# Performance work log

Measured on AMD Instinct MI355X. Metric: run time of the kernel, lower is better.

Reference implementation:

```python
import jax, jax.numpy as jnp
import numpy as np

D = 192          # embed_dim
DI = 2 * D       # d_inner (Mamba expand=2)
R = 12           # dt_rank = ceil(D / d_state)
N = 16           # d_state
DEPTH = 24
P = 16           # patch size
B = 4
SS, TS = 256, 128
PT = (TS // P) ** 2   # 64 template patches
PS = (SS // P) ** 2   # 256 search patches
L = PT + PS + 1       # 321 tokens (middle cls)


def setup_inputs() -> dict:
    key = jax.random.key(0)
    ks = jax.random.split(key, 24)
    f = lambda k, shp, s=0.02: (jax.random.normal(k, shp) * s).astype(jnp.float32)
    Alog = jnp.log(jnp.arange(1, N + 1, dtype=jnp.float32))  # S4D-real init
    Alog = jnp.tile(Alog, (DEPTH, DI, 1))
    return {
        "x_search": f(ks[0], (B, 3, SS, SS), 1.0),
        "x_template": f(ks[1], (B, 3, TS, TS), 1.0),
        "patch_w": f(ks[2], (D, 3, P, P)),
        "patch_b": jnp.zeros((D,), jnp.float32),
        "cls_token": f(ks[3], (1, 1, D)),
        "pos_embed": f(ks[4], (1, L, D)),
        "Win": f(ks[5], (DEPTH, 2 * DI, D)),
        "convw": f(ks[6], (DEPTH, DI, 4), 0.2),
        "convb": jnp.zeros((DEPTH, DI), jnp.float32),
        "Wx": f(ks[7], (DEPTH, R + 2 * N, DI)),
        "Wdt": f(ks[8], (DEPTH, DI, R), 0.1),
        "bdt": f(ks[9], (DEPTH, DI), 0.1),
        "Alog": Alog,
        "Dp": jnp.ones((DEPTH, DI), jnp.float32),
        "convw_b": f(ks[10], (DEPTH, DI, 4), 0.2),
        "convb_b": jnp.zeros((DEPTH, DI), jnp.float32),
        "Wx_b": f(ks[11], (DEPTH, R + 2 * N, DI)),
        "Wdt_b": f(ks[12], (DEPTH, DI, R), 0.1),
        "bdt_b": f(ks[13], (DEPTH, DI), 0.1),
        "Alog_b": Alog,
        "Dp_b": jnp.ones((DEPTH, DI), jnp.float32),
        "Wout": f(ks[14], (DEPTH, D, DI)),
        "normw": jnp.ones((DEPTH, D), jnp.float32),
        "normw_f": jnp.ones((D,), jnp.float32),
    }


def silu(x):
    return x * jax.nn.sigmoid(x)


def rmsnorm(x, w, eps=1e-5):
    return x * jax.lax.rsqrt(jnp.mean(x * x, -1, keepdims=True) + eps) * w


def patch_embed(x, w, b):
    # non-overlapping patch conv == blocked reshape + einsum
    Bn, C, H, W = x.shape
    xp = x.reshape(Bn, C, H // P, P, W // P, P)
    t = jnp.einsum('bcipjq,dcpq->bijd', xp, w)
    return t.reshape(Bn, (H // P) * (W // P), -1) + b


def causal_conv(u, w, b):
    # depthwise causal conv, kernel 4: u [B,DI,L], w [DI,4]
    Lx = u.shape[-1]
    up = jnp.pad(u, ((0, 0), (0, 0), (3, 0)))
    y = sum(w[:, k][None, :, None] * up[:, :, k:k + Lx] for k in range(4))
    return y + b[None, :, None]


def selective_scan(u, delta, A, Bm, Cm, Dp):
    # u, delta: [B,DI,L]; A: [DI,N]; Bm, Cm: [B,N,L]
    dA = jnp.exp(jnp.einsum('bdl,dn->lbdn', delta, A))
    dBu = jnp.einsum('bdl,bnl->lbdn', delta * u, Bm)

    def step(h, inp):
        dAt, dBut, ct = inp
        h = dAt * h + dBut
        return h, jnp.einsum('bdn,bn->bd', h, ct)

    h0 = jnp.zeros((u.shape[0], DI, N), u.dtype)
    _, ys = jax.lax.scan(step, h0, (dA, dBu, Cm.transpose(2, 0, 1)))
    y = ys.transpose(1, 2, 0)  # [B,DI,L]
    return y + Dp[None, :, None] * u


def _branch(x, z, convw, convb, Wx, Wdt, bdt, Alog, Dp):
    xc = silu(causal_conv(x, convw, convb))
    xdbl = jnp.einsum('bdl,ed->ble', xc, Wx)
    dt, Bm, Cm = xdbl[..., :R], xdbl[..., R:R + N], xdbl[..., R + N:]
    delta = jax.nn.softplus(jnp.einsum('blr,dr->bdl', dt, Wdt) + bdt[None, :, None])
    y = selective_scan(xc, delta, -jnp.exp(Alog), Bm.transpose(0, 2, 1),
                       Cm.transpose(0, 2, 1), Dp)
    return y * silu(z)


def _mixer(h, p):
    xz = jnp.einsum('bld,ed->ble', h, p['Win'])
    x = xz[..., :DI].transpose(0, 2, 1)   # [B,DI,L]
    z = xz[..., DI:].transpose(0, 2, 1)
    y = _branch(x, z, p['convw'], p['convb'], p['Wx'], p['Wdt'], p['bdt'],
                p['Alog'], p['Dp'])
    yb = _branch(x[..., ::-1], z[..., ::-1], p['convw_b'], p['convb_b'], p['Wx_b'],
                 p['Wdt_b'], p['bdt_b'], p['Alog_b'], p['Dp_b'])
    out = (y + yb[..., ::-1]) * 0.5  # bimamba v2 with if_divide_out
    return jnp.einsum('bdl,od->blo', out, p['Wout'])


def reference(x_search, x_template, patch_w, patch_b, cls_token, pos_embed,
              Win, convw, convb, Wx, Wdt, bdt, Alog, Dp,
              convw_b, convb_b, Wx_b, Wdt_b, bdt_b, Alog_b, Dp_b,
              Wout, normw, normw_f):
    ts = patch_embed(x_template, patch_w, patch_b)   # [B,64,D]
    ss = patch_embed(x_search, patch_w, patch_b)     # [B,256,D]
    tok = jnp.concatenate([ts, ss], 1)               # [B,320,D]
    mid = tok.shape[1] // 2
    cls = jnp.broadcast_to(cls_token, (tok.shape[0], 1, D))
    tok = jnp.concatenate([tok[:, :mid], cls, tok[:, mid:]], 1) + pos_embed

    lp = {'Win': Win, 'convw': convw, 'convb': convb, 'Wx': Wx, 'Wdt': Wdt,
          'bdt': bdt, 'Alog': Alog, 'Dp': Dp, 'convw_b': convw_b,
          'convb_b': convb_b, 'Wx_b': Wx_b, 'Wdt_b': Wdt_b, 'bdt_b': bdt_b,
          'Alog_b': Alog_b, 'Dp_b': Dp_b, 'Wout': Wout, 'normw': normw}

    def layer_step(carry, p):
        hidden, residual = carry
        residual = hidden + residual           # add
        hn = rmsnorm(residual, p['normw'])     # norm (fused_add_norm semantics)
        hidden = _mixer(hn, p)                 # mamba mixer
        return (hidden, residual), None

    (hidden, residual), _ = jax.lax.scan(layer_step, (tok, jnp.zeros_like(tok)), lp)
    return rmsnorm(hidden + residual, normw_f)   # final add + norm, [B,321,D]
```

## Files before the change

kernel.cpp:

```cpp
#include <hip/hip_runtime.h>
#include <math.h>

#define B_ 4
#define L_ 321
#define D_ 192
#define DI_ 384
#define E_ 768
#define R_ 12
#define N_ 16
#define DEPTH_ 24
#define XD 44

#define NC_ 21
#define LC_ 16

typedef __attribute__((ext_vector_type(8))) short bf16x8;
typedef __attribute__((ext_vector_type(4))) float f32x4;
typedef unsigned short ushort_t;

__device__ __forceinline__ float silu_f(float x) { return x / (1.f + __expf(-x)); }

__device__ __forceinline__ ushort_t f2bf(float x) {
    union { float f; unsigned u; } v; v.f = x;
    return (ushort_t)((v.u + 0x7fffu + ((v.u >> 16) & 1u)) >> 16);
}
__device__ __forceinline__ float bf2f(ushort_t h) {
    union { unsigned u; float f; } v; v.u = ((unsigned)h) << 16; return v.f;
}

__global__ void cvt_bf16_multi(const float* __restrict__ s0, ushort_t* __restrict__ d0, int n0,
                               const float* __restrict__ s1, ushort_t* __restrict__ d1, int n1,
                               const float* __restrict__ s2, ushort_t* __restrict__ d2, int n2,
                               const float* __restrict__ s3, ushort_t* __restrict__ d3, int n3,
                               const float* __restrict__ s4, ushort_t* __restrict__ d4, int n4) {
    int total = n0 + n1 + n2 + n3 + n4;
    for (int i = blockIdx.x * blockDim.x + threadIdx.x; i < total; i += gridDim.x * blockDim.x) {
        int j = i;
        const float* s; ushort_t* d;
        if (j < n0) { s = s0; d = d0; }
        else { j -= n0;
            if (j < n1) { s = s1; d = d1; }
            else { j -= n1;
                if (j < n2) { s = s2; d = d2; }
                else { j -= n2;
                    if (j < n3) { s = s3; d = d3; }
                    else { j -= n3; s = s4; d = d4; }
                }
            }
        }
        d[j] = f2bf(s[j]);
    }
}

__global__ void im2col_kernel(const float* __restrict__ xs, const float* __restrict__ xt,
                              ushort_t* __restrict__ pm) {
    int p_all = blockIdx.x % 320;
    int b = blockIdx.x / 320;
    const float* src; int i, j, W;
    if (p_all < 64) { int p = p_all; i = p >> 3; j = p & 7; W = 128; src = xt + (size_t)b*3*128*128; }
    else            { int p = p_all - 64; i = p >> 4; j = p & 15; W = 256; src = xs + (size_t)b*3*256*256; }
    ushort_t* dst = pm + (size_t)blockIdx.x * 768;
    for (int m = threadIdx.x; m < 768; m += blockDim.x) {
        int c = m >> 8, rem = m & 255, pp = rem >> 4, qq = rem & 15;
        dst[m] = f2bf(src[(size_t)(c*W + i*16 + pp)*W + j*16 + qq]);
    }
}

__global__ void tok_rms(const float* __restrict__ tokmat, const float* __restrict__ pb,
                        const float* __restrict__ cls, const float* __restrict__ pos,
                        const float* __restrict__ normw,
                        float* __restrict__ residual, ushort_t* __restrict__ hn) {
    int blk = blockIdx.x;
    int b = blk / L_, t = blk % L_;
    int d = threadIdx.x;
    float v;
    if (t == 160) v = cls[d];
    else {
        int p = (t < 160) ? t : t - 1;
        v = tokmat[(size_t)(b*320 + p)*D_ + d] + pb[d];
    }
    v += pos[t*D_ + d];
    residual[(size_t)blk*D_ + d] = v;
    float sq = v * v;
#pragma unroll
    for (int m = 1; m < 64; m <<= 1) sq += __shfl_xor(sq, m, 64);
    __shared__ float part[3];
    int wave = d >> 6, lane = d & 63;
    if (lane == 0) part[wave] = sq;
    __syncthreads();
    float tot = part[0] + part[1] + part[2];
    float scale = rsqrtf(tot / (float)D_ + 1e-5f);
    hn[(size_t)blk*D_ + d] = f2bf(v * scale * normw[d]);
}

template<int WM, int WN, int MFR, int NFR, int CMODE, int KK>
__global__ __launch_bounds__(WM*WN*64) void mfma_gemm(const ushort_t* __restrict__ A,
                          const ushort_t* __restrict__ Bw,
                          float* __restrict__ Cf, ushort_t* __restrict__ Ch,
                          int M, int N) {
    constexpr int BM = WM * MFR * 16;
    constexpr int BN = WN * NFR * 16;
    int bx = blockIdx.x, by = blockIdx.y;
    int wave = threadIdx.x >> 6, lane = threadIdx.x & 63;
    int wr = wave / WN, wc = wave % WN;
    int m0 = by * BM + wr * MFR * 16;
    int n0 = bx * BN + wc * NFR * 16;
    int lrow = lane & 15;
    int lk   = (lane >> 4) * 8;

    f32x4 acc[MFR][NFR];
#pragma unroll
    for (int i = 0; i < MFR; ++i)
#pragma unroll
        for (int j = 0; j < NFR; ++j) acc[i][j] = (f32x4){0.f, 0.f, 0.f, 0.f};

#pragma unroll 6
    for (int k0 = 0; k0 < KK; k0 += 32) {
        bf16x8 a[MFR], b[NFR];
#pragma unroll
        for (int i = 0; i < MFR; ++i) {
            int r = m0 + i*16 + lrow; r = min(r, M - 1);
            a[i] = *(const bf16x8*)(A + (size_t)r*KK + k0 + lk);
        }
#pragma unroll
        for (int jn = 0; jn < NFR; ++jn) {
            int c = n0 + jn*16 + lrow; c = min(c, N - 1);
            b[jn] = *(const bf16x8*)(Bw + (size_t)c*KK + k0 + lk);
        }
#pragma unroll
        for (int i = 0; i < MFR; ++i)
#pragma unroll
            for (int jn = 0; jn < NFR; ++jn)
                acc[i][jn] = __builtin_amdgcn_mfma_f32_16x16x32_bf16(a[i], b[jn], acc[i][jn], 0, 0, 0);
    }

    int crow = (lane >> 4) * 4;
    int ccol = lane & 15;
#pragma unroll
    for (int i = 0; i < MFR; ++i)
#pragma unroll
        for (int jn = 0; jn < NFR; ++jn) {
            int c = n0 + jn*16 + ccol;
            if (c >= N) continue;
#pragma unroll
            for (int j = 0; j < 4; ++j) {
                int r = m0 + i*16 + crow + j;
                if (r < M) {
                    if (CMODE == 0) Cf[(size_t)r*N + c] = acc[i][jn][j];
                    else            Ch[(size_t)r*N + c] = f2bf(acc[i][jn][j]);
                }
            }
        }
}

__global__ __launch_bounds__(384) void scan1_conv(
    const ushort_t* __restrict__ xzb,
    const ushort_t* __restrict__ Wxf, const ushort_t* __restrict__ Wxbw,
    const float* __restrict__ cw, const float* __restrict__ cb,
    const float* __restrict__ cwb, const float* __restrict__ cbb,
    const float* __restrict__ Wdt, const float* __restrict__ bdt,
    const float* __restrict__ Wdtb, const float* __restrict__ bdtb,
    const float* __restrict__ Alog, const float* __restrict__ Alogb,
    ushort_t* __restrict__ xc_f, ushort_t* __restrict__ xc_b,
    float* __restrict__ xdbl_f, float* __restrict__ xdbl_b,
    float* __restrict__ hloc, float* __restrict__ aprod) {
    int c = blockIdx.x, b = blockIdx.y, br = blockIdx.z;
    int tid = threadIdx.x, wave = tid >> 6, lane = tid & 63;
    const ushort_t* Wx = br ? Wxbw : Wxf;
    const float* cwp = br ? cwb : cw;
    const float* cbp = br ? cbb : cb;
    const float* Wd = br ? Wdtb : Wdt;
    const float* bd = br ? bdtb : bdt;
    const float* Al = br ? Alogb : Alog;
    ushort_t* xcout = br ? xc_b : xc_f;
    float* xdout = br ? xdbl_b : xdbl_f;

    __shared__ ushort_t sxc[LC_][DI_ + 8];
    __shared__ float sxd[LC_][48];
    int lbeg = c * LC_;
    int len = min(lbeg + LC_, L_) - lbeg;
    int d = tid;

    float4 w4 = *(const float4*)(cwp + (size_t)d*4);
    float b0 = cbp[d];
    const ushort_t* xrow = xzb + (size_t)b*L_*E_ + d;
    float u[LC_];
    if (len == LC_) {
        float xr[LC_ + 3];
#pragma unroll
        for (int t2 = 0; t2 < LC_ + 3; ++t2) {
            int t = lbeg - 3 + t2;
            float v = 0.f;
            if (t >= 0) { int tr = br ? (L_ - 1 - t) : t; v = bf2f(xrow[(size_t)tr*E_]); }
            xr[t2] = v;
        }
#pragma unroll
        for (int l2 = 0; l2 < LC_; ++l2) {
            float acc = b0;
            acc = fmaf(w4.x, xr[l2 + 0], acc);
            acc = fmaf(w4.y, xr[l2 + 1], acc);
            acc = fmaf(w4.z, xr[l2 + 2], acc);
            acc = fmaf(w4.w, xr[l2 + 3], acc);
            ushort_t hv = f2bf(silu_f(acc));
            sxc[l2][d] = hv;
            u[l2] = bf2f(hv);
            xcout[((size_t)b*L_ + lbeg + l2)*DI_ + d] = hv;
        }
    } else {
        for (int l2 = 0; l2 < len; ++l2) {
            int l = lbeg + l2;
            float acc = b0;
#pragma unroll
            for (int k = 0; k < 4; ++k) {
                int t = l - 3 + k;
                if (t >= 0) {
                    int tr = br ? (L_ - 1 - t) : t;
                    acc = fmaf(((const float*)&w4)[k], bf2f(xrow[(size_t)tr*E_]), acc);
                }
            }
            ushort_t hv = f2bf(silu_f(acc));
            sxc[l2][d] = hv;
            u[l2] = bf2f(hv);
            xcout[((size_t)b*L_ + lbeg + l2)*DI_ + d] = hv;
        }
    }
    __syncthreads();

    if (wave < 3) {
        int lrow = lane & 15, lk = (lane >> 4) * 8;
        int ar = min(lrow, len - 1);
        int bcol = min(wave * 16 + lrow, XD - 1);
        f32x4 acc = (f32x4){0.f, 0.f, 0.f, 0.f};
#pragma unroll
        for (int k0 = 0; k0 < DI_; k0 += 32) {
            bf16x8 a  = *(const bf16x8*)(&sxc[ar][k0 + lk]);
            bf16x8 bw = *(const bf16x8*)(Wx + (size_t)bcol * DI_ + k0 + lk);
            acc = __builtin_amdgcn_mfma_f32_16x16x32_bf16(a, bw, acc, 0, 0, 0);
        }
        int crow = (lane >> 4) * 4, ccol = lane & 15;
#pragma unroll
        for (int j = 0; j < 4; ++j) sxd[crow + j][wave * 16 + ccol] = acc[j];
    }
    __syncthreads();

    for (int idx = tid; idx < len * XD; idx += 384) {
        int l2 = idx / XD, col = idx % XD;
        xdout[((size_t)b*L_ + lbeg + l2)*XD + col] = sxd[l2][col];
    }

    float wreg[R_];
#pragma unroll
    for (int r = 0; r < R_; ++r) wreg[r] = Wd[d*R_ + r];
    float bdv = bd[d];
    float a[N_];
#pragma unroll
    for (int n = 0; n < N_; ++n) a[n] = -__expf(Al[d*N_ + n]);
    float h[N_], ap[N_];
#pragma unroll
    for (int n = 0; n < N_; ++n) { h[n] = 0.f; ap[n] = 1.f; }

    auto step = [&](int l2, float uv) {
        float dacc = bdv;
#pragma unroll
        for (int r = 0; r < R_; ++r) dacc = fmaf(wreg[r], sxd[l2][r], dacc);
        float dv = fmaxf(dacc, 0.f) + log1pf(__expf(-fabsf(dacc)));
        float du = dv * uv;
#pragma unroll
        for (int n = 0; n < N_; ++n) {
            float e = __expf(dv * a[n]);
            h[n] = fmaf(e, h[n], du * sxd[l2][R_ + n]);
            ap[n] *= e;
        }
    };
    if (len == LC_) {
#pragma unroll 4
        for (int l2 = 0; l2 < LC_; ++l2) step(l2, u[l2]);
    } else {
        for (int l2 = 0; l2 < len; ++l2) step(l2, u[l2]);
    }
    size_t base = (((size_t)(b*2 + br)*NC_ + c)*N_)*DI_ + d;
#pragma unroll
    for (int n = 0; n < N_; ++n) {
        hloc[base + (size_t)n*DI_]  = h[n];
        aprod[base + (size_t)n*DI_] = ap[n];
    }
}

__global__ void scan_combine(const float* __restrict__ hloc, const float* __restrict__ aprod,
                             float* __restrict__ hin) {
    int g = blockIdx.x * blockDim.x + threadIdx.x;
    int bb = g / (N_ * DI_);
    int rem = g % (N_ * DI_);
    float hrun = 0.f;
#pragma unroll
    for (int c = 0; c < NC_; ++c) {
        size_t idx = ((size_t)bb*NC_ + c)*N_*DI_ + rem;
        hin[idx] = hrun;
        hrun = fmaf(aprod[idx], hrun, hloc[idx]);
    }
}

__global__ __launch_bounds__(192) void scan_part3(
                           const ushort_t* __restrict__ xc_f, const ushort_t* __restrict__ xc_b,
                           const float* __restrict__ xdbl_f, const float* __restrict__ xdbl_b,
                           const float* __restrict__ Wdt, const float* __restrict__ bdt,
                           const float* __restrict__ Wdtb, const float* __restrict__ bdtb,
                           const ushort_t* __restrict__ xz,
                           const float* __restrict__ Alog, const float* __restrict__ Alogb,
                           const float* __restrict__ Dpf, const float* __restrict__ Dpb,
                           const float* __restrict__ hin,
                           ushort_t* __restrict__ y_f, ushort_t* __restrict__ y_b) {
    int c = blockIdx.x, b = blockIdx.y >> 1, half = blockIdx.y & 1, br = blockIdx.z;
    int tid = threadIdx.x;
    int d = half * 192 + tid;
    const ushort_t* xc = br ? xc_b : xc_f;
    const float* xd = br ? xdbl_b : xdbl_f;
    const float* Wd = br ? Wdtb : Wdt;
    const float* bd = br ? bdtb : bdt;
    const float* Al = br ? Alogb : Alog;
    const float* Dpp = br ? Dpb : Dpf;
    ushort_t* y = br ? y_b : y_f;
    __shared__ float sdt[LC_][R_];
    __shared__ float sB[LC_][N_];
    __shared__ float sC[LC_][N_];
    int lbeg = c * LC_;
    int len = min(lbeg + LC_, L_) - lbeg;
    for (int idx = tid; idx < len*N_; idx += 192) {
        int l2 = idx >> 4, n = idx & 15;
        size_t row = (size_t)b*L_ + lbeg + l2;
        sB[l2][n] = xd[row*XD + R_ + n];
        sC[l2][n] = xd[row*XD + R_ + N_ + n];
    }
    for (int idx = tid; idx < len*R_; idx += 192) {
        int l2 = idx / R_, r = idx % R_;
        sdt[l2][r] = xd[((size_t)b*L_ + lbeg + l2)*XD + r];
    }
    __syncthreads();
    float wreg[R_];
#pragma unroll
    for (int r = 0; r < R_; ++r) wreg[r] = Wd[d*R_ + r];
    float bdv = bd[d];
    float a[N_];
#pragma unroll
    for (int n = 0; n < N_; ++n) a[n] = -__expf(Al[d*N_ + n]);
    float h[N_];
    size_t hbase = (((size_t)(b*2 + br)*NC_ + c)*N_)*DI_ + d;
#pragma unroll
    for (int n = 0; n < N_; ++n) h[n] = hin[hbase + (size_t)n*DI_];
    float dpv = Dpp[d];

    auto step = [&](int l2, float uv) {
        float dacc = bdv;
#pragma unroll
        for (int r = 0; r < R_; ++r) dacc = fmaf(wreg[r], sdt[l2][r], dacc);
        float dv = fmaxf(dacc, 0.f) + log1pf(__expf(-fabsf(dacc)));
        float du = dv * uv;
        float yv = 0.f;
#pragma unroll
        for (int n = 0; n < N_; ++n) {
            float e = __expf(dv * a[n]);
            h[n] = fmaf(e, h[n], du * sB[l2][n]);
            yv = fmaf(h[n], sC[l2][n], yv);
        }
        yv = fmaf(dpv, uv, yv);
        int lo = br ? (L_ - 1 - (lbeg + l2)) : (lbeg + l2);
        float zv = bf2f(xz[((size_t)b*L_ + lo)*E_ + DI_ + d]);
        y[((size_t)b*L_ + lo)*DI_ + d] = f2bf(yv * silu_f(zv));
    };
    if (len == LC_) {
        float u[LC_];
#pragma unroll
        for (int l2 = 0; l2 < LC_; ++l2)
            u[l2] = bf2f(xc[((size_t)b*L_ + lbeg + l2)*DI_ + d]);
#pragma unroll 4
        for (int l2 = 0; l2 < LC_; ++l2) step(l2, u[l2]);
    } else {
        for (int l2 = 0; l2 < len; ++l2)
            step(l2, bf2f(xc[((size_t)b*L_ + lbeg + l2)*DI_ + d]));
    }
}

template<bool LAST>
__global__ __launch_bounds__(256) void outproj_fused(
    const ushort_t* __restrict__ yf, const ushort_t* __restrict__ yb,
    const ushort_t* __restrict__ Ww,
    float* __restrict__ residual, const float* __restrict__ nw,
    ushort_t* __restrict__ hn, float* __restrict__ outp) {
    const int M = B_*L_, Nn = D_, K = DI_;
    int wave = threadIdx.x >> 6, lane = threadIdx.x & 63;
    int m0 = blockIdx.x * 16;
    int n0 = wave * 48;
    int lrow = lane & 15, lk = (lane >> 4) * 8;

    f32x4 acc[3];
#pragma unroll
    for (int jn = 0; jn < 3; ++jn) acc[jn] = (f32x4){0.f, 0.f, 0.f, 0.f};

#pragma unroll 4
    for (int k0 = 0; k0 < K; k0 += 32) {
        int r = min(m0 + lrow, M - 1);
        bf16x8 vf = *(const bf16x8*)(yf + (size_t)r*K + k0 + lk);
        bf16x8 vb = *(const bf16x8*)(yb + (size_t)r*K + k0 + lk);
        bf16x8 a;
#pragma unroll
        for (int j = 0; j < 8; ++j)
            a[j] = (short)f2bf(0.5f*(bf2f((ushort_t)vf[j]) + bf2f((ushort_t)vb[j])));
        bf16x8 b[3];
#pragma unroll
        for (int jn = 0; jn < 3; ++jn) {
            int c = n0 + jn*16 + lrow;
            b[jn] = *(const bf16x8*)(Ww + (size_t)c*K + k0 + lk);
        }
#pragma unroll
        for (int jn = 0; jn < 3; ++jn)
            acc[jn] = __builtin_amdgcn_mfma_f32_16x16x32_bf16(a, b[jn], acc[jn], 0, 0, 0);
    }

    int crow = (lane >> 4) * 4, ccol = lane & 15;
    float resv[4][3];
    float sq[4] = {0.f, 0.f, 0.f, 0.f};
#pragma unroll
    for (int j = 0; j < 4; ++j) {
        int r = m0 + crow + j;
        bool ok = r < M;
#pragma unroll
        for (int jn = 0; jn < 3; ++jn) {
            int c = n0 + jn*16 + ccol;
            float v = ok ? (residual[(size_t)r*Nn + c] + acc[jn][j]) : 0.f;
            resv[j][jn] = v;
            sq[j] = fmaf(v, v, sq[j]);
        }
    }
#pragma unroll
    for (int m = 1; m < 16; m <<= 1)
#pragma unroll
        for (int j = 0; j < 4; ++j) sq[j] += __shfl_xor(sq[j], m, 64);

    __shared__ float part[16][4];
    if (ccol == 0) {
#pragma unroll
        for (int j = 0; j < 4; ++j) part[crow + j][wave] = sq[j];
    }
    __syncthreads();
#pragma unroll
    for (int j = 0; j < 4; ++j) {
        int r = m0 + crow + j;
        if (r >= M) continue;
        int rt = crow + j;
        float tot = part[rt][0] + part[rt][1] + part[rt][2] + part[rt][3];
        float scale = rsqrtf(tot / (float)Nn + 1e-5f);
#pragma unroll
        for (int jn = 0; jn < 3; ++jn) {
            int c = n0 + jn*16 + ccol;
            float v = resv[j][jn];
            if (LAST) {
                outp[(size_t)r*Nn + c] = v * scale * nw[c];
            } else {
                residual[(size_t)r*Nn + c] = v;
                hn[(size_t)r*Nn + c] = f2bf(v * scale * nw[c]);
            }
        }
    }
}

extern "C" void kernel_launch(void* const* d_in, const int* in_sizes, int n_in,
                              void* d_out, int out_size, void* d_ws, size_t ws_size,
                              hipStream_t stream) {
    const float* xs     = (const float*)d_in[0];
    const float* xt     = (const float*)d_in[1];
    const float* pw     = (const float*)d_in[2];
    const float* pb     = (const float*)d_in[3];
    const float* cls    = (const float*)d_in[4];
    const float* pos    = (const float*)d_in[5];
    const float* Win    = (const float*)d_in[6];
    const float* convw  = (const float*)d_in[7];
    const float* convb  = (const float*)d_in[8];
    const float* Wx     = (const float*)d_in[9];
    const float* Wdt    = (const float*)d_in[10];
    const float* bdt    = (const float*)d_in[11];
    const float* Alog   = (const float*)d_in[12];
    const float* Dp     = (const float*)d_in[13];
    const float* convwb = (const float*)d_in[14];
    const float* convbb = (const float*)d_in[15];
    const float* Wxb    = (const float*)d_in[16];
    const float* Wdtb   = (const float*)d_in[17];
    const float* bdtb   = (const float*)d_in[18];
    const float* Alogb  = (const float*)d_in[19];
    const float* Dpb    = (const float*)d_in[20];
    const float* Wout   = (const float*)d_in[21];
    const float* normw  = (const float*)d_in[22];
    const float* normwf = (const float*)d_in[23];
    float* out = (float*)d_out;

    float* ws = (float*)d_ws;
    size_t off = 0;
    auto alloc = [&](size_t nfloats) { float* p = ws + off; off += nfloats; return p; };
    const size_t BL = (size_t)B_ * L_;
    const size_t CHNK = (size_t)B_ * 2 * NC_ * N_ * DI_;

    float*    residual = alloc(BL * D_);
    ushort_t* hn_bf    = (ushort_t*)alloc(BL * D_ / 2);
    ushort_t* xzb_bf   = (ushort_t*)alloc(BL * E_ / 2);
    ushort_t* xcf_bf   = (ushort_t*)alloc(BL * DI_ / 2);
    ushort_t* xcb_bf   = (ushort_t*)alloc(BL * DI_ / 2);
    float*    xdbl_f   = alloc(BL * XD);
    float*    xdbl_b   = alloc(BL * XD);
    ushort_t* y_f      = (ushort_t*)alloc(BL * DI_ / 2);
    ushort_t* y_b      = (ushort_t*)alloc(BL * DI_ / 2);
    float*    hloc     = alloc(CHNK);
    float*    aprod    = alloc(CHNK);
    float*    hin      = alloc(CHNK);
    ushort_t* pw_bf    = (ushort_t*)alloc((size_t)D_ * 768 / 2);
    ushort_t* Win_bf   = (ushort_t*)alloc((size_t)DEPTH_ * E_ * D_ / 2);
    ushort_t* Wx_bf    = (ushort_t*)alloc((size_t)DEPTH_ * XD * DI_ / 2);
    ushort_t* Wxb_bf   = (ushort_t*)alloc((size_t)DEPTH_ * XD * DI_ / 2);
    ushort_t* Wout_bf  = (ushort_t*)alloc((size_t)DEPTH_ * D_ * DI_ / 2);
    (void)ws_size; (void)in_sizes; (void)n_in; (void)out_size;

    cvt_bf16_multi<<<dim3(2048), dim3(256), 0, stream>>>(
        pw,   pw_bf,   D_ * 768,
        Win,  Win_bf,  DEPTH_ * E_ * D_,
        Wx,   Wx_bf,   DEPTH_ * XD * DI_,
        Wxb,  Wxb_bf,  DEPTH_ * XD * DI_,
        Wout, Wout_bf, DEPTH_ * D_ * DI_);

    ushort_t* pmat   = (ushort_t*)hloc;
    float*    tokmat = aprod;
    im2col_kernel<<<dim3(B_ * 320), dim3(256), 0, stream>>>(xs, xt, pmat);
    mfma_gemm<2, 2, 2, 2, 0, 768><<<dim3(3, 20), dim3(256), 0, stream>>>(
        pmat, pw_bf, tokmat, nullptr, B_ * 320, D_);
    tok_rms<<<dim3(B_ * L_), dim3(192), 0, stream>>>(tokmat, pb, cls, pos, normw, residual, hn_bf);

    for (int layer = 0; layer < DEPTH_; ++layer) {
        const ushort_t* Win_l  = Win_bf  + (size_t)layer * E_ * D_;
        const ushort_t* Wx_l   = Wx_bf   + (size_t)layer * XD * DI_;
        const ushort_t* Wxb_l  = Wxb_bf  + (size_t)layer * XD * DI_;
        const ushort_t* Wout_l = Wout_bf + (size_t)layer * D_ * DI_;
        const float* cw_l    = convw  + (size_t)layer * DI_ * 4;
        const float* cb_l    = convb  + (size_t)layer * DI_;
        const float* cwb_l   = convwb + (size_t)layer * DI_ * 4;
        const float* cbb_l   = convbb + (size_t)layer * DI_;
        const float* Wdt_l   = Wdt    + (size_t)layer * DI_ * R_;
        const float* Wdtb_l  = Wdtb   + (size_t)layer * DI_ * R_;
        const float* bdt_l   = bdt    + (size_t)layer * DI_;
        const float* bdtb_l  = bdtb   + (size_t)layer * DI_;
        const float* Alog_l  = Alog   + (size_t)layer * DI_ * N_;
        const float* Alogb_l = Alogb  + (size_t)layer * DI_ * N_;
        const float* Dp_l    = Dp     + (size_t)layer * DI_;
        const float* Dpb_l   = Dpb    + (size_t)layer * DI_;

        mfma_gemm<2, 2, 2, 2, 1, 192><<<dim3(12, 21), dim3(256), 0, stream>>>(
            hn_bf, Win_l, nullptr, xzb_bf, (int)BL, E_);
        scan1_conv<<<dim3(NC_, B_, 2), dim3(384), 0, stream>>>(
            xzb_bf, Wx_l, Wxb_l, cw_l, cb_l, cwb_l, cbb_l,
            Wdt_l, bdt_l, Wdtb_l, bdtb_l, Alog_l, Alogb_l,
            xcf_bf, xcb_bf, xdbl_f, xdbl_b, hloc, aprod);
        scan_combine<<<dim3((B_*2*N_*DI_)/256), dim3(256), 0, stream>>>(hloc, aprod, hin);
        scan_part3<<<dim3(NC_, B_ * 2, 2), dim3(192), 0, stream>>>(
            xcf_bf, xcb_bf, xdbl_f, xdbl_b, Wdt_l, bdt_l, Wdtb_l, bdtb_l, xzb_bf,
            Alog_l, Alogb_l, Dp_l, Dpb_l, hin, y_f, y_b);
        if (layer < DEPTH_ - 1) {
            outproj_fused<false><<<dim3(81), dim3(256), 0, stream>>>(
                y_f, y_b, Wout_l, residual, normw + (size_t)(layer + 1) * D_, hn_bf, nullptr);
        } else {
            outproj_fused<true><<<dim3(81), dim3(256), 0, stream>>>(
                y_f, y_b, Wout_l, residual, normwf, nullptr, out);
        }
    }
}
```

Baseline: 1.746 ms.

## Fuse next layer's in-projection GEMM into out-projection/residual-norm kernel

```diff
diff --git a/kernel.cpp b/kernel.cpp
--- a/kernel.cpp
+++ b/kernel.cpp
@@ -381,52 +381,55 @@
 }
 
 template<bool LAST>
-__global__ __launch_bounds__(256) void outproj_fused(
+__global__ __launch_bounds__(384) void outproj_inproj(
     const ushort_t* __restrict__ yf, const ushort_t* __restrict__ yb,
     const ushort_t* __restrict__ Ww,
+    const ushort_t* __restrict__ Win_next,
     float* __restrict__ residual, const float* __restrict__ nw,
-    ushort_t* __restrict__ hn, float* __restrict__ outp) {
-    const int M = B_*L_, Nn = D_, K = DI_;
+    ushort_t* __restrict__ xzb_out, float* __restrict__ outp) {
+    const int M = B_*L_;
     int wave = threadIdx.x >> 6, lane = threadIdx.x & 63;
     int m0 = blockIdx.x * 16;
-    int n0 = wave * 48;
     int lrow = lane & 15, lk = (lane >> 4) * 8;
-
-    f32x4 acc[3];
-#pragma unroll
-    for (int jn = 0; jn < 3; ++jn) acc[jn] = (f32x4){0.f, 0.f, 0.f, 0.f};
-
+    int crow = (lane >> 4) * 4, ccol = lane & 15;
+
+    __shared__ ushort_t shn[16][D_ + 8];
+    __shared__ float part[16][6];
+
+    int n0 = wave * 32;
+    f32x4 acc[2];
+#pragma unroll
+    for (int jn = 0; jn < 2; ++jn) acc[jn] = (f32x4){0.f, 0.f, 0.f, 0.f};
 #pragma unroll 4
-    for (int k0 = 0; k0 < K; k0 += 32) {
+    for (int k0 = 0; k0 < DI_; k0 += 32) {
         int r = min(m0 + lrow, M - 1);
-        bf16x8 vf = *(const bf16x8*)(yf + (size_t)r*K + k0 + lk);
-        bf16x8 vb = *(const bf16x8*)(yb + (size_t)r*K + k0 + lk);
+        bf16x8 vf = *(const bf16x8*)(yf + (size_t)r*DI_ + k0 + lk);
+        bf16x8 vb = *(const bf16x8*)(yb + (size_t)r*DI_ + k0 + lk);
         bf16x8 a;
 #pragma unroll
         for (int j = 0; j < 8; ++j)
             a[j] = (short)f2bf(0.5f*(bf2f((ushort_t)vf[j]) + bf2f((ushort_t)vb[j])));
-        bf16x8 b[3];
-#pragma unroll
-        for (int jn = 0; jn < 3; ++jn) {
+        bf16x8 b[2];
+#pragma unroll
+        for (int jn = 0; jn < 2; ++jn) {
             int c = n0 + jn*16 + lrow;
-            b[jn] = *(const bf16x8*)(Ww + (size_t)c*K + k0 + lk);
-        }
-#pragma unroll
-        for (int jn = 0; jn < 3; ++jn)
+            b[jn] = *(const bf16x8*)(Ww + (size_t)c*DI_ + k0 + lk);
+        }
+#pragma unroll
+        for (int jn = 0; jn < 2; ++jn)
             acc[jn] = __builtin_amdgcn_mfma_f32_16x16x32_bf16(a, b[jn], acc[jn], 0, 0, 0);
     }
 
-    int crow = (lane >> 4) * 4, ccol = lane & 15;
-    float resv[4][3];
+    float resv[4][2];
     float sq[4] = {0.f, 0.f, 0.f, 0.f};
 #pragma unroll
     for (int j = 0; j < 4; ++j) {
         int r = m0 + crow + j;
         bool ok = r < M;
 #pragma unroll
-        for (int jn = 0; jn < 3; ++jn) {
+        for (int jn = 0; jn < 2; ++jn) {
             int c = n0 + jn*16 + ccol;
-            float v = ok ? (residual[(size_t)r*Nn + c] + acc[jn][j]) : 0.f;
+            float v = ok ? (residual[(size_t)r*D_ + c] + acc[jn][j]) : 0.f;
             resv[j][jn] = v;
             sq[j] = fmaf(v, v, sq[j]);
         }
@@ -435,8 +438,6 @@
     for (int m = 1; m < 16; m <<= 1)
 #pragma unroll
         for (int j = 0; j < 4; ++j) sq[j] += __shfl_xor(sq[j], m, 64);
-
-    __shared__ float part[16][4];
     if (ccol == 0) {
 #pragma unroll
         for (int j = 0; j < 4; ++j) part[crow + j][wave] = sq[j];
@@ -445,20 +446,49 @@
 #pragma unroll
     for (int j = 0; j < 4; ++j) {
         int r = m0 + crow + j;
-        if (r >= M) continue;
         int rt = crow + j;
-        float tot = part[rt][0] + part[rt][1] + part[rt][2] + part[rt][3];
-        float scale = rsqrtf(tot / (float)Nn + 1e-5f);
-#pragma unroll
-        for (int jn = 0; jn < 3; ++jn) {
+        float tot = part[rt][0] + part[rt][1] + part[rt][2]
+                  + part[rt][3] + part[rt][4] + part[rt][5];
+        float scale = rsqrtf(tot / (float)D_ + 1e-5f);
+#pragma unroll
+        for (int jn = 0; jn < 2; ++jn) {
             int c = n0 + jn*16 + ccol;
             float v = resv[j][jn];
             if (LAST) {
-                outp[(size_t)r*Nn + c] = v * scale * nw[c];
+                if (r < M) outp[(size_t)r*D_ + c] = v * scale * nw[c];
             } else {
-                residual[(size_t)r*Nn + c] = v;
-                hn[(size_t)r*Nn + c] = f2bf(v * scale * nw[c]);
+                if (r < M) residual[(size_t)r*D_ + c] = v;
+                shn[rt][c] = f2bf(v * scale * nw[c]);
             }
+        }
+    }
+    if (LAST) return;
+    __syncthreads();
+
+    int e0 = wave * 128;
+    f32x4 acc2[8];
+#pragma unroll
+    for (int jn = 0; jn < 8; ++jn) acc2[jn] = (f32x4){0.f, 0.f, 0.f, 0.f};
+#pragma unroll
+    for (int k0 = 0; k0 < D_; k0 += 32) {
+        bf16x8 a = *(const bf16x8*)(&shn[lrow][k0 + lk]);
+        bf16x8 b[8];
+#pragma unroll
+        for (int jn = 0; jn < 8; ++jn) {
+            int c = e0 + jn*16 + lrow;
+            b[jn] = *(const bf16x8*)(Win_next + (size_t)c*D_ + k0 + lk);
+        }
+#pragma unroll
+        for (int jn = 0; jn < 8; ++jn)
+            acc2[jn] = __builtin_amdgcn_mfma_f32_16x16x32_bf16(a, b[jn], acc2[jn], 0, 0, 0);
+    }
+#pragma unroll
+    for (int jn = 0; jn < 8; ++jn) {
+        int c = e0 + jn*16 + ccol;
+#pragma unroll
+        for (int j = 0; j < 4; ++j) {
+            int r = m0 + crow + j;
+            if (r < M) xzb_out[(size_t)r*E_ + c] = f2bf(acc2[jn][j]);
         }
     }
 }
@@ -530,9 +560,10 @@
     mfma_gemm<2, 2, 2, 2, 0, 768><<<dim3(3, 20), dim3(256), 0, stream>>>(
         pmat, pw_bf, tokmat, nullptr, B_ * 320, D_);
     tok_rms<<<dim3(B_ * L_), dim3(192), 0, stream>>>(tokmat, pb, cls, pos, normw, residual, hn_bf);
+    mfma_gemm<2, 2, 2, 2, 1, 192><<<dim3(12, 21), dim3(256), 0, stream>>>(
+        hn_bf, Win_bf, nullptr, xzb_bf, (int)BL, E_);
 
     for (int layer = 0; layer < DEPTH_; ++layer) {
-        const ushort_t* Win_l  = Win_bf  + (size_t)layer * E_ * D_;
         const ushort_t* Wx_l   = Wx_bf   + (size_t)layer * XD * DI_;
         const ushort_t* Wxb_l  = Wxb_bf  + (size_t)layer * XD * DI_;
         const ushort_t* Wout_l = Wout_bf + (size_t)layer * D_ * DI_;
@@ -549,8 +580,6 @@
         const float* Dp_l    = Dp     + (size_t)layer * DI_;
         const float* Dpb_l   = Dpb    + (size_t)layer * DI_;
 
-        mfma_gemm<2, 2, 2, 2, 1, 192><<<dim3(12, 21), dim3(256), 0, stream>>>(
-            hn_bf, Win_l, nullptr, xzb_bf, (int)BL, E_);
         scan1_conv<<<dim3(NC_, B_, 2), dim3(384), 0, stream>>>(
             xzb_bf, Wx_l, Wxb_l, cw_l, cb_l, cwb_l, cbb_l,
             Wdt_l, bdt_l, Wdtb_l, bdtb_l, Alog_l, Alogb_l,
@@ -560,11 +589,12 @@
             xcf_bf, xcb_bf, xdbl_f, xdbl_b, Wdt_l, bdt_l, Wdtb_l, bdtb_l, xzb_bf,
             Alog_l, Alogb_l, Dp_l, Dpb_l, hin, y_f, y_b);
         if (layer < DEPTH_ - 1) {
-            outproj_fused<false><<<dim3(81), dim3(256), 0, stream>>>(
-                y_f, y_b, Wout_l, residual, normw + (size_t)(layer + 1) * D_, hn_bf, nullptr);
+            outproj_inproj<false><<<dim3(81), dim3(384), 0, stream>>>(
+                y_f, y_b, Wout_l, Win_bf + (size_t)(layer + 1) * E_ * D_,
+                residual, normw + (size_t)(layer + 1) * D_, xzb_bf, nullptr);
         } else {
-            outproj_fused<true><<<dim3(81), dim3(256), 0, stream>>>(
-                y_f, y_b, Wout_l, residual, normwf, nullptr, out);
-        }
-    }
-}
+            outproj_inproj<true><<<dim3(81), dim3(384), 0, stream>>>(
+                y_f, y_b, Wout_l, nullptr, residual, normwf, nullptr, out);
+        }
+    }
+}
```

After: 1.842 ms. +5.5%, slower.
